# Optimization experiments

Measured on AMD Instinct MI355X. Metric: run time of the kernel, lower is better.

Reference implementation:

```python
import jax, jax.numpy as jnp
import numpy as np

D_NODE, D_EDGE, D_HEAD = 256, 128, 32
LN_EPS = 1e-5


def setup_inputs() -> dict:
    key = jax.random.key(0)
    ks = jax.random.split(key, 10)
    B, N = 1, 512
    s_node = 1.0 / np.sqrt(D_NODE)
    s_hh = 1.0 / np.sqrt(D_HEAD * D_HEAD)
    return {
        "node": jax.random.normal(ks[0], (B, N, D_NODE), dtype=jnp.float32),
        "edge": jax.random.normal(ks[1], (B, N, N, D_EDGE), dtype=jnp.float32),
        "ln_w": jnp.ones((D_NODE,), dtype=jnp.float32),
        "ln_b": jnp.zeros((D_NODE,), dtype=jnp.float32),
        "w_left": jax.random.normal(ks[2], (D_NODE, D_HEAD), dtype=jnp.float32) * s_node,
        "b_left": jax.random.normal(ks[3], (D_HEAD,), dtype=jnp.float32) * 0.02,
        "w_right": jax.random.normal(ks[4], (D_NODE, D_HEAD), dtype=jnp.float32) * s_node,
        "b_right": jax.random.normal(ks[5], (D_HEAD,), dtype=jnp.float32) * 0.02,
        "w_out": jax.random.normal(ks[6], (D_HEAD * D_HEAD, D_EDGE), dtype=jnp.float32) * s_hh,
        "b_out": jax.random.normal(ks[7], (D_EDGE,), dtype=jnp.float32) * 0.02,
    }


def reference(node, edge, ln_w, ln_b, w_left, b_left, w_right, b_right, w_out, b_out):
    # LayerNorm over d_node
    mu = jnp.mean(node, axis=-1, keepdims=True)
    var = jnp.mean(jnp.square(node - mu), axis=-1, keepdims=True)
    x = (node - mu) * jax.lax.rsqrt(var + LN_EPS) * ln_w + ln_b

    left = x @ w_left + b_left    # [B, N, d_head]
    right = x @ w_right + b_right  # [B, N, d_head]

    # Outer product flattened over (i,j) then projected to d_edge.
    # Fused: reshape w_out to [i, j, e] and contract directly, avoiding the
    # explicit [B, N, N, d_head*d_head] intermediate (same math as
    # einsum('bni,bmj->bnmij').flatten(-2) @ w_out).
    w3 = w_out.reshape(D_HEAD, D_HEAD, D_EDGE)
    out = jnp.einsum("bni,bmj,ije->bnme", left, right, w3) + b_out
    return out + edge
```

## Files before the change

kernel.cpp:

```cpp
#include <hip/hip_runtime.h>

#define D_NODE 256
#define D_EDGE 128
#define D_HEAD 32
#define NN 512

typedef float f4v __attribute__((ext_vector_type(4)));

__global__ __launch_bounds__(256) void ln_proj_kernel(
    const float* __restrict__ node, const float* __restrict__ ln_w,
    const float* __restrict__ ln_b, const float* __restrict__ w_left,
    const float* __restrict__ b_left, const float* __restrict__ w_right,
    const float* __restrict__ b_right, float* __restrict__ left,
    float* __restrict__ right) {
  __shared__ float xs[D_NODE];
  __shared__ float red[10];
  __shared__ float part[4][64];
  const int n = blockIdx.x;
  const int t = threadIdx.x;
  float v = node[n * D_NODE + t];
  float s = v, ss = v * v;
#pragma unroll
  for (int o = 32; o > 0; o >>= 1) {
    s += __shfl_down(s, o);
    ss += __shfl_down(ss, o);
  }
  if ((t & 63) == 0) {
    red[t >> 6] = s;
    red[4 + (t >> 6)] = ss;
  }
  __syncthreads();
  if (t == 0) {
    float S = red[0] + red[1] + red[2] + red[3];
    float SS = red[4] + red[5] + red[6] + red[7];
    float mu = S * (1.0f / D_NODE);
    float var = SS * (1.0f / D_NODE) - mu * mu;
    red[8] = mu;
    red[9] = rsqrtf(var + 1e-5f);
  }
  __syncthreads();
  const float mu = red[8], rs = red[9];
  xs[t] = (v - mu) * rs * ln_w[t] + ln_b[t];
  __syncthreads();
  {
    const int col = t & 63;
    const int q = t >> 6;
    const int c = col & 31;
    const float* w = (col < 32) ? w_left : w_right;
    float acc = 0.f;
    const int d0 = q * 64;
#pragma unroll 8
    for (int d = d0; d < d0 + 64; ++d) acc = fmaf(xs[d], w[d * D_HEAD + c], acc);
    part[q][col] = acc;
  }
  __syncthreads();
  if (t < 64) {
    const int c = t & 31;
    const bool isL = (t < 32);
    float acc = part[0][t] + part[1][t] + part[2][t] + part[3][t] +
                (isL ? b_left[c] : b_right[c]);
    (isL ? left : right)[n * D_HEAD + c] = acc;
  }
}

__global__ __launch_bounds__(256) void rw_kernel(
    const float* __restrict__ right, const float* __restrict__ w_out,
    float* __restrict__ tmp) {
  const int m0 = blockIdx.x * 4;
  const int i = blockIdx.y * 8 + (threadIdx.x >> 5);
  const int e4 = threadIdx.x & 31;
  const float4* wp = (const float4*)(w_out + i * D_HEAD * D_EDGE) + e4;
  const float* r = right + m0 * D_HEAD;
  float4 a0 = {0, 0, 0, 0}, a1 = {0, 0, 0, 0}, a2 = {0, 0, 0, 0},
         a3 = {0, 0, 0, 0};
#pragma unroll
  for (int j = 0; j < D_HEAD; ++j) {
    const float4 w4 = wp[j * (D_EDGE / 4)];
    const float r0 = r[j], r1 = r[32 + j], r2 = r[64 + j], r3 = r[96 + j];
    a0.x = fmaf(r0, w4.x, a0.x); a0.y = fmaf(r0, w4.y, a0.y);
    a0.z = fmaf(r0, w4.z, a0.z); a0.w = fmaf(r0, w4.w, a0.w);
    a1.x = fmaf(r1, w4.x, a1.x); a1.y = fmaf(r1, w4.y, a1.y);
    a1.z = fmaf(r1, w4.z, a1.z); a1.w = fmaf(r1, w4.w, a1.w);
    a2.x = fmaf(r2, w4.x, a2.x); a2.y = fmaf(r2, w4.y, a2.y);
    a2.z = fmaf(r2, w4.z, a2.z); a2.w = fmaf(r2, w4.w, a2.w);
    a3.x = fmaf(r3, w4.x, a3.x); a3.y = fmaf(r3, w4.y, a3.y);
    a3.z = fmaf(r3, w4.z, a3.z); a3.w = fmaf(r3, w4.w, a3.w);
  }
  ((float4*)(tmp + ((m0 + 0) * D_HEAD + i) * D_EDGE))[e4] = a0;
  ((float4*)(tmp + ((m0 + 1) * D_HEAD + i) * D_EDGE))[e4] = a1;
  ((float4*)(tmp + ((m0 + 2) * D_HEAD + i) * D_EDGE))[e4] = a2;
  ((float4*)(tmp + ((m0 + 3) * D_HEAD + i) * D_EDGE))[e4] = a3;
}

__global__ __launch_bounds__(256) void fuse_kernel(
    const float* __restrict__ left, const float* __restrict__ tmp,
    const float* __restrict__ b_out, const float* __restrict__ edge,
    float* __restrict__ out) {
  __shared__ float tl[2 * D_HEAD * D_EDGE];
  const int m0 = blockIdx.x * 2;
  const int t = threadIdx.x;
  {
    const float4* ts = (const float4*)(tmp + m0 * D_HEAD * D_EDGE);
    float4* td = (float4*)tl;
#pragma unroll
    for (int k = 0; k < 8; ++k) td[t + 256 * k] = ts[t + 256 * k];
  }
  const int lane = t & 63;
  const int wv = __builtin_amdgcn_readfirstlane(t >> 6);
  const int e4 = lane & 31;
  const int mh = lane >> 5;
  const int n0 = blockIdx.y * 64 + wv * 16;
  const float4 be = ((const float4*)b_out)[e4];
  const float* tb = tl + mh * (D_HEAD * D_EDGE) + e4 * 4;
  const float4* edge4 = (const float4*)edge;
  float4* out4 = (float4*)out;
  const int rowstr = NN * (D_EDGE / 4);
  const int base = (n0 * NN + m0) * (D_EDGE / 4) + lane;

  float4 eb[2][8];
#pragma unroll
  for (int r = 0; r < 8; ++r) eb[0][r] = edge4[base + r * rowstr];
  __syncthreads();

#pragma unroll
  for (int g = 0; g < 2; ++g) {
    const int cur = g & 1;
    const int gb = base + g * 8 * rowstr;
    if (g < 1) {
#pragma unroll
      for (int r = 0; r < 8; ++r)
        eb[cur ^ 1][r] = edge4[gb + (8 + r) * rowstr];
    }
    float4 acc[8];
#pragma unroll
    for (int r = 0; r < 8; ++r) acc[r] = be;
    const float* lp = left + (n0 + g * 8) * D_HEAD;
#pragma unroll 4
    for (int i = 0; i < D_HEAD; ++i) {
      const float4 tv = *(const float4*)(tb + i * D_EDGE);
#pragma unroll
      for (int r = 0; r < 8; ++r) {
        const float l = lp[r * D_HEAD + i];
        acc[r].x = fmaf(l, tv.x, acc[r].x);
        acc[r].y = fmaf(l, tv.y, acc[r].y);
        acc[r].z = fmaf(l, tv.z, acc[r].z);
        acc[r].w = fmaf(l, tv.w, acc[r].w);
      }
    }
#pragma unroll
    for (int r = 0; r < 8; ++r) {
      acc[r].x += eb[cur][r].x;
      acc[r].y += eb[cur][r].y;
      acc[r].z += eb[cur][r].z;
      acc[r].w += eb[cur][r].w;
      __builtin_nontemporal_store(*(const f4v*)&acc[r],
                                  (f4v*)(out4 + gb + r * rowstr));
    }
  }
}

extern "C" void kernel_launch(void* const* d_in, const int* in_sizes, int n_in,
                              void* d_out, int out_size, void* d_ws, size_t ws_size,
                              hipStream_t stream) {
  const float* node    = (const float*)d_in[0];
  const float* edge    = (const float*)d_in[1];
  const float* ln_w    = (const float*)d_in[2];
  const float* ln_b    = (const float*)d_in[3];
  const float* w_left  = (const float*)d_in[4];
  const float* b_left  = (const float*)d_in[5];
  const float* w_right = (const float*)d_in[6];
  const float* b_right = (const float*)d_in[7];
  const float* w_out   = (const float*)d_in[8];
  const float* b_out   = (const float*)d_in[9];
  float* out = (float*)d_out;

  float* left  = (float*)d_ws;
  float* right = left + NN * D_HEAD;
  float* tmp   = right + NN * D_HEAD;

  ln_proj_kernel<<<NN, 256, 0, stream>>>(node, ln_w, ln_b, w_left, b_left,
                                         w_right, b_right, left, right);
  rw_kernel<<<dim3(NN / 4, 4), 256, 0, stream>>>(right, w_out, tmp);
  fuse_kernel<<<dim3(NN / 2, 8), 256, 0, stream>>>(left, tmp, b_out, edge, out);
}
```

Baseline: 269.8 us.

## Retile fuse kernel with XCD-aware block mapping and direct tmp reads

The fuse kernel drops its shared-memory staging of tmp and reads tmp straight from global memory, relying on cache hits. Each block now covers 16 m columns by 32 n rows instead of 2 m by 64 n, with every wave looping over 8 m pairs while double-buffering edge loads. Block ids are remapped so that blocks on the same XCD share m ranges and therefore tmp slices in L2. This removes the LDS copy and barrier, but every wave now issues more global loads for tmp and the grid shrinks to 512 blocks.

Measured after the change: 298.7 us. 10.7% more time.

```diff
diff --git a/kernel.cpp b/kernel.cpp
--- a/kernel.cpp
+++ b/kernel.cpp
@@ -96,48 +96,50 @@
     const float* __restrict__ left, const float* __restrict__ tmp,
     const float* __restrict__ b_out, const float* __restrict__ edge,
     float* __restrict__ out) {
-  __shared__ float tl[2 * D_HEAD * D_EDGE];
-  const int m0 = blockIdx.x * 2;
+  const int bid = blockIdx.x;
+  const int xcd = bid & 7;
+  const int idx = bid >> 3;
+  const int mr = xcd * 4 + (idx & 3);
+  const int ng = idx >> 2;
   const int t = threadIdx.x;
-  {
-    const float4* ts = (const float4*)(tmp + m0 * D_HEAD * D_EDGE);
-    float4* td = (float4*)tl;
-#pragma unroll
-    for (int k = 0; k < 8; ++k) td[t + 256 * k] = ts[t + 256 * k];
-  }
   const int lane = t & 63;
-  const int wv = __builtin_amdgcn_readfirstlane(t >> 6);
+  const int wv = t >> 6;
   const int e4 = lane & 31;
   const int mh = lane >> 5;
-  const int n0 = blockIdx.y * 64 + wv * 16;
+  const int m0 = mr * 16;
+  const int n0 = ng * 32 + wv * 8;
+
   const float4 be = ((const float4*)b_out)[e4];
-  const float* tb = tl + mh * (D_HEAD * D_EDGE) + e4 * 4;
   const float4* edge4 = (const float4*)edge;
+  const float4* tmp4 = (const float4*)tmp;
   float4* out4 = (float4*)out;
-  const int rowstr = NN * (D_EDGE / 4);
-  const int base = (n0 * NN + m0) * (D_EDGE / 4) + lane;
+  const float* lp = left + n0 * D_HEAD;
+
+  int base[8];
+#pragma unroll
+  for (int r = 0; r < 8; ++r)
+    base[r] = (((n0 + r) * NN + m0 + mh) << 5) + e4;
+  const int tbase = (((m0 + mh) * D_HEAD) << 5) + e4;
 
   float4 eb[2][8];
 #pragma unroll
-  for (int r = 0; r < 8; ++r) eb[0][r] = edge4[base + r * rowstr];
-  __syncthreads();
+  for (int r = 0; r < 8; ++r) eb[0][r] = edge4[base[r]];
 
 #pragma unroll
-  for (int g = 0; g < 2; ++g) {
-    const int cur = g & 1;
-    const int gb = base + g * 8 * rowstr;
-    if (g < 1) {
+  for (int mp = 0; mp < 8; ++mp) {
+    const int cur = mp & 1;
+    if (mp < 7) {
 #pragma unroll
       for (int r = 0; r < 8; ++r)
-        eb[cur ^ 1][r] = edge4[gb + (8 + r) * rowstr];
+        eb[cur ^ 1][r] = edge4[base[r] + (mp + 1) * 64];
     }
     float4 acc[8];
 #pragma unroll
     for (int r = 0; r < 8; ++r) acc[r] = be;
-    const float* lp = left + (n0 + g * 8) * D_HEAD;
+    const int tb = tbase + mp * 2048;
 #pragma unroll 4
     for (int i = 0; i < D_HEAD; ++i) {
-      const float4 tv = *(const float4*)(tb + i * D_EDGE);
+      const float4 tv = tmp4[tb + (i << 5)];
 #pragma unroll
       for (int r = 0; r < 8; ++r) {
         const float l = lp[r * D_HEAD + i];
@@ -154,7 +156,7 @@
       acc[r].z += eb[cur][r].z;
       acc[r].w += eb[cur][r].w;
       __builtin_nontemporal_store(*(const f4v*)&acc[r],
-                                  (f4v*)(out4 + gb + r * rowstr));
+                                  (f4v*)(out4 + base[r] + mp * 64));
     }
   }
 }
@@ -181,5 +183,5 @@
   ln_proj_kernel<<<NN, 256, 0, stream>>>(node, ln_w, ln_b, w_left, b_left,
                                          w_right, b_right, left, right);
   rw_kernel<<<dim3(NN / 4, 4), 256, 0, stream>>>(right, w_out, tmp);
-  fuse_kernel<<<dim3(NN / 2, 8), 256, 0, stream>>>(left, tmp, b_out, edge, out);
+  fuse_kernel<<<dim3(512), 256, 0, stream>>>(left, tmp, b_out, edge, out);
 }
```
